# Kernel optimization log

Measured on AMD Instinct MI355X. Metric: run time of the kernel, lower is better.

## Reference

```python
import jax, jax.numpy as jnp
import numpy as np

N_NODES = 50000
N_EDGES = 400000
NODE_FEAT = 32
HIDDEN = 256
ACTION_DIM = 6
NUM_GRAPHS = 64


def setup_inputs() -> dict:
    key = jax.random.key(0)
    ks = jax.random.split(key, 9)
    x = jax.random.normal(ks[0], (N_NODES, NODE_FEAT), dtype=jnp.float32)
    edge_index = jax.random.randint(ks[1], (2, N_EDGES), 0, N_NODES, dtype=jnp.int32)
    batch = jnp.sort(jax.random.randint(ks[2], (N_NODES,), 0, NUM_GRAPHS, dtype=jnp.int32))
    # GCNConv weights (PyG stores Linear without bias + separate bias term;
    # here W is [in, out] so h = x @ W)
    s1 = 1.0 / np.sqrt(NODE_FEAT)
    s2 = 1.0 / np.sqrt(HIDDEN)
    W1 = jax.random.uniform(ks[3], (NODE_FEAT, HIDDEN), jnp.float32, -s1, s1)
    b1 = jnp.zeros((HIDDEN,), jnp.float32)
    W2 = jax.random.uniform(ks[4], (HIDDEN, HIDDEN), jnp.float32, -s2, s2)
    b2 = jnp.zeros((HIDDEN,), jnp.float32)
    Wf = jax.random.uniform(ks[5], (HIDDEN, 2 * ACTION_DIM), jnp.float32, -s2, s2)
    bf = jax.random.uniform(ks[6], (2 * ACTION_DIM,), jnp.float32, -s2, s2)
    return {"x": x, "edge_index": edge_index, "batch": batch,
            "W1": W1, "b1": b1, "W2": W2, "b2": b2, "Wf": Wf, "bf": bf}


def gcn_conv(x, src, dst, deg_inv_sqrt, W, b, num_nodes):
    # PyG GCNConv: h = x @ W, messages h[src] * norm scattered to dst, + bias.
    h = x @ W  # [N, out]
    norm = deg_inv_sqrt[src] * deg_inv_sqrt[dst]  # [E+N]
    msgs = h[src] * norm[:, None]  # [E+N, out]  (dominant memory traffic)
    out = jax.ops.segment_sum(msgs, dst, num_segments=num_nodes)
    return out + b


def reference(x, edge_index, batch, W1, b1, W2, b2, Wf, bf):
    num_nodes = x.shape[0]
    loop = jnp.arange(num_nodes, dtype=edge_index.dtype)
    src = jnp.concatenate([edge_index[0], loop])  # self-loops, PyG default
    dst = jnp.concatenate([edge_index[1], loop])
    deg = jax.ops.segment_sum(jnp.ones_like(dst, dtype=x.dtype), dst,
                              num_segments=num_nodes)  # >=1 due to self-loops
    deg_inv_sqrt = jax.lax.rsqrt(deg)

    h = jax.nn.relu(gcn_conv(x, src, dst, deg_inv_sqrt, W1, b1, num_nodes))
    h = jax.nn.relu(gcn_conv(h, src, dst, deg_inv_sqrt, W2, b2, num_nodes))

    # global_mean_pool over graph ids
    sums = jax.ops.segment_sum(h, batch, num_segments=NUM_GRAPHS)
    counts = jax.ops.segment_sum(jnp.ones((num_nodes,), x.dtype), batch,
                                 num_segments=NUM_GRAPHS)
    pooled = sums / jnp.maximum(counts, 1.0)[:, None]  # [G, HIDDEN]

    mls = pooled @ Wf + bf  # [G, 2*ACTION_DIM]
    mean, log_std = jnp.split(mls, 2, axis=-1)
    std = jnp.exp(jnp.clip(log_std, -20.0, 2.0))
    return mean, std
```

## Files before the change

kernel.cpp:

```cpp
#include <hip/hip_runtime.h>
#include <math.h>

#define NN 50000
#define FEAT 32
#define HID 256
#define NGRAPH 64
#define CAP 48

typedef __attribute__((ext_vector_type(8))) short bfrag;
typedef __attribute__((ext_vector_type(8))) unsigned short u16x8;
typedef __attribute__((ext_vector_type(4))) float f32x4;

__device__ __forceinline__ float bf2f(unsigned short u) {
    union { unsigned int i; float f; } v; v.i = ((unsigned int)u) << 16; return v.f;
}
__device__ __forceinline__ unsigned short f2bf(float f) {
    union { float f; unsigned int i; } v; v.f = f;
    unsigned int r = v.i + 0x7fffu + ((v.i >> 16) & 1u);
    return (unsigned short)(r >> 16);
}

__device__ __forceinline__ void pack_w(const float* __restrict__ W,
                                       unsigned short* __restrict__ Wp, int K, int o) {
    int j    = o & 7;
    int lane = (o >> 3) & 63;
    int rest = o >> 9;
    int nst  = K >> 5;
    int ks   = rest & (nst - 1);
    int nb   = rest / nst;
    int n = nb * 16 + (lane & 15);
    int k = ks * 32 + (lane >> 4) * 8 + j;
    Wp[o] = f2bf(W[(size_t)k * HID + n]);
}

__global__ void k_prep(float4* __restrict__ zp, int n16,
                       const float* __restrict__ W1, const float* __restrict__ W2,
                       unsigned short* __restrict__ W1p, unsigned short* __restrict__ W2p) {
    int i = blockIdx.x * blockDim.x + threadIdx.x;
    if (i < n16) zp[i] = make_float4(0.f, 0.f, 0.f, 0.f);
    if (i < FEAT * HID) pack_w(W1, W1p, FEAT, i);
    int o2 = i - FEAT * HID;
    if (o2 >= 0 && o2 < HID * HID) pack_w(W2, W2p, HID, o2);
}

__global__ void k_setup(const int* __restrict__ src, const int* __restrict__ dst,
                        const int* __restrict__ batch,
                        int* __restrict__ counter, unsigned short* __restrict__ csr,
                        int* __restrict__ starts, int E, int N) {
    int e = blockIdx.x * blockDim.x + threadIdx.x;
    if (e < E) {
        int d = dst[e];
        int p = atomicAdd(&counter[d], 1);
        if (p < CAP) csr[(size_t)d * CAP + p] = (unsigned short)src[e];
    }
    if (e < N) {
        int b = batch[e];
        int prev = (e == 0) ? -1 : batch[e - 1];
        if (b != prev) {
            for (int g = prev + 1; g <= b; ++g) starts[g] = e;
        }
        if (e == N - 1) {
            for (int g = b + 1; g <= NGRAPH; ++g) starts[g] = N;
        }
    }
}

__global__ void k_aggx(const float* __restrict__ x, const int* __restrict__ cnt,
                       const unsigned short* __restrict__ csr,
                       unsigned short* __restrict__ out, int N) {
    int node = blockIdx.x * 8 + (threadIdx.x >> 5);
    if (node >= N) return;
    int col = threadIdx.x & 31;
    int ecnt = cnt[node];
    float dn = rsqrtf((float)(ecnt + 1));
    int e = ecnt > CAP ? CAP : ecnt;
    const unsigned short* lst = &csr[(size_t)node * CAP];

    float acc = x[(size_t)node * FEAT + col] * dn;
    int i = 0;
    for (; i + 8 <= e; i += 8) {
        u16x8 s = *(const u16x8*)&lst[i];
        float vs[8];
#pragma unroll
        for (int j = 0; j < 8; ++j) {
            int sj = (int)s[j];
            vs[j] = x[(size_t)sj * FEAT + col] * rsqrtf((float)(cnt[sj] + 1));
        }
        acc += ((vs[0] + vs[1]) + (vs[2] + vs[3])) + ((vs[4] + vs[5]) + (vs[6] + vs[7]));
    }
    for (; i + 4 <= e; i += 4) {
        float vs[4];
#pragma unroll
        for (int j = 0; j < 4; ++j) {
            int sj = (int)lst[i + j];
            vs[j] = x[(size_t)sj * FEAT + col] * rsqrtf((float)(cnt[sj] + 1));
        }
        acc += (vs[0] + vs[1]) + (vs[2] + vs[3]);
    }
    for (; i < e; ++i) {
        int sj = (int)lst[i];
        acc += x[(size_t)sj * FEAT + col] * rsqrtf((float)(cnt[sj] + 1));
    }
    out[(size_t)node * FEAT + col] = f2bf(acc * dn);
}

__global__ void k_aggh(const unsigned short* __restrict__ hp, const int* __restrict__ cnt,
                       const unsigned short* __restrict__ csr,
                       unsigned short* __restrict__ outp, int N) {
    int panel = blockIdx.x & 7;
    int node = (blockIdx.x >> 3) * 64 + (threadIdx.x >> 2);
    if (node >= N) return;
    int c0 = (threadIdx.x & 3) * 8;
    const unsigned short* h = hp + (size_t)panel * N * 32;
    unsigned short* out = outp + (size_t)panel * N * 32;

    int ecnt = cnt[node];
    float dn = rsqrtf((float)(ecnt + 1));
    int e = ecnt > CAP ? CAP : ecnt;
    const unsigned short* lst = &csr[(size_t)node * CAP];

    bfrag sv = *(const bfrag*)&h[(size_t)node * 32 + c0];
    float a[8];
#pragma unroll
    for (int j = 0; j < 8; ++j) a[j] = bf2f((unsigned short)sv[j]);

    int i = 0;
    for (; i + 8 <= e; i += 8) {
        u16x8 s = *(const u16x8*)&lst[i];
        bfrag w0 = *(const bfrag*)&h[(size_t)s[0] * 32 + c0];
        bfrag w1 = *(const bfrag*)&h[(size_t)s[1] * 32 + c0];
        bfrag w2 = *(const bfrag*)&h[(size_t)s[2] * 32 + c0];
        bfrag w3 = *(const bfrag*)&h[(size_t)s[3] * 32 + c0];
        bfrag w4 = *(const bfrag*)&h[(size_t)s[4] * 32 + c0];
        bfrag w5 = *(const bfrag*)&h[(size_t)s[5] * 32 + c0];
        bfrag w6 = *(const bfrag*)&h[(size_t)s[6] * 32 + c0];
        bfrag w7 = *(const bfrag*)&h[(size_t)s[7] * 32 + c0];
#pragma unroll
        for (int j = 0; j < 8; ++j) {
            a[j] += ((bf2f((unsigned short)w0[j]) + bf2f((unsigned short)w1[j]))
                   + (bf2f((unsigned short)w2[j]) + bf2f((unsigned short)w3[j])))
                  + ((bf2f((unsigned short)w4[j]) + bf2f((unsigned short)w5[j]))
                   + (bf2f((unsigned short)w6[j]) + bf2f((unsigned short)w7[j])));
        }
    }
    for (; i + 4 <= e; i += 4) {
        bfrag w0 = *(const bfrag*)&h[(size_t)lst[i]     * 32 + c0];
        bfrag w1 = *(const bfrag*)&h[(size_t)lst[i + 1] * 32 + c0];
        bfrag w2 = *(const bfrag*)&h[(size_t)lst[i + 2] * 32 + c0];
        bfrag w3 = *(const bfrag*)&h[(size_t)lst[i + 3] * 32 + c0];
#pragma unroll
        for (int j = 0; j < 8; ++j)
            a[j] += (bf2f((unsigned short)w0[j]) + bf2f((unsigned short)w1[j]))
                  + (bf2f((unsigned short)w2[j]) + bf2f((unsigned short)w3[j]));
    }
    for (; i < e; ++i) {
        bfrag w = *(const bfrag*)&h[(size_t)lst[i] * 32 + c0];
#pragma unroll
        for (int j = 0; j < 8; ++j) a[j] += bf2f((unsigned short)w[j]);
    }
    bfrag o;
#pragma unroll
    for (int j = 0; j < 8; ++j) o[j] = (short)f2bf(a[j] * dn);
    *(bfrag*)&out[(size_t)node * 32 + c0] = o;
}

__global__ __launch_bounds__(256, 4)
void k_mmf(const unsigned short* __restrict__ A, const unsigned short* __restrict__ Wp,
           const float* __restrict__ bias, const int* __restrict__ cnt,
           unsigned short* __restrict__ C, int M) {
    __shared__ unsigned short lds[64 * 264];
    const int K = FEAT;
    int tid  = threadIdx.x;
    int lane = tid & 63;
    int wid  = tid >> 6;
    int l15  = lane & 15;
    int lq   = lane >> 4;
    int row0 = blockIdx.x * 64;

    const int P = K + 8;
    {
        int flat = tid * 8;
        int row = flat >> 5;
        int col = flat & 31;
        bfrag v = {0, 0, 0, 0, 0, 0, 0, 0};
        int gr = row0 + row;
        if (gr < M) v = *(const bfrag*)&A[(size_t)gr * K + col];
        *(bfrag*)&lds[row * P + col] = v;
    }
    __syncthreads();

    f32x4 acc[4][4];
#pragma unroll
    for (int mi = 0; mi < 4; ++mi)
#pragma unroll
        for (int ni = 0; ni < 4; ++ni) acc[mi][ni] = (f32x4){0.f, 0.f, 0.f, 0.f};

    bfrag fb[4];
#pragma unroll
    for (int ni = 0; ni < 4; ++ni) {
        size_t off = (((size_t)(wid * 4 + ni)) * 64 + lane) * 8;
        fb[ni] = *(const bfrag*)&Wp[off];
    }
    bfrag fa[4];
#pragma unroll
    for (int mi = 0; mi < 4; ++mi)
        fa[mi] = *(const bfrag*)&lds[(mi * 16 + l15) * P + lq * 8];
#pragma unroll
    for (int mi = 0; mi < 4; ++mi)
#pragma unroll
        for (int ni = 0; ni < 4; ++ni)
            acc[mi][ni] = __builtin_amdgcn_mfma_f32_16x16x32_bf16(fb[ni], fa[mi], acc[mi][ni], 0, 0, 0);

    float4 bv[4];
#pragma unroll
    for (int ni = 0; ni < 4; ++ni)
        bv[ni] = *(const float4*)&bias[(wid * 4 + ni) * 16 + lq * 4];
    float sv[4];
#pragma unroll
    for (int mi = 0; mi < 4; ++mi) {
        int gr = row0 + mi * 16 + l15;
        sv[mi] = (gr < M) ? rsqrtf((float)(cnt[gr] + 1)) : 0.f;
    }

    __syncthreads();
#pragma unroll
    for (int mi = 0; mi < 4; ++mi) {
#pragma unroll
        for (int ni = 0; ni < 4; ++ni) {
            const float* bp = (const float*)&bv[ni];
            ushort4 o;
            o.x = f2bf(fmaxf(acc[mi][ni][0] + bp[0], 0.f) * sv[mi]);
            o.y = f2bf(fmaxf(acc[mi][ni][1] + bp[1], 0.f) * sv[mi]);
            o.z = f2bf(fmaxf(acc[mi][ni][2] + bp[2], 0.f) * sv[mi]);
            o.w = f2bf(fmaxf(acc[mi][ni][3] + bp[3], 0.f) * sv[mi]);
            *(ushort4*)&lds[(mi * 16 + l15) * 264 + (wid * 4 + ni) * 16 + lq * 4] = o;
        }
    }
    __syncthreads();

#pragma unroll
    for (int i = 0; i < 8; ++i) {
        int F = (i * 256 + tid) * 8;
        int row = F >> 8;
        int col = F & 255;
        int gr = row0 + row;
        if (gr < M) {
            bfrag v = *(const bfrag*)&lds[row * 264 + col];
            *(bfrag*)&C[((size_t)(col >> 5) * M + gr) * 32 + (col & 31)] = v;
        }
    }
}

__global__ __launch_bounds__(256, 4)
void k_mmfp(const unsigned short* __restrict__ A, const unsigned short* __restrict__ Wp,
            const float* __restrict__ bias, const int* __restrict__ batch,
            float* __restrict__ pooled, int M) {
    __shared__ unsigned short lds[64 * 264];
    __shared__ int bshare[64];
    const int K = HID;
    int tid  = threadIdx.x;
    int lane = tid & 63;
    int wid  = tid >> 6;
    int l15  = lane & 15;
    int lq   = lane >> 4;
    int row0 = blockIdx.x * 64;

    if (tid < 64) {
        int gr = row0 + tid;
        bshare[tid] = (gr < M) ? batch[gr] : -1;
    }

    const int P = K + 8;
    for (int it = 0; it < 8; ++it) {
        int flat = (it * 256 + tid) * 8;
        int row = flat >> 8;
        int col = flat & 255;
        bfrag v = {0, 0, 0, 0, 0, 0, 0, 0};
        int gr = row0 + row;
        if (gr < M) v = *(const bfrag*)&A[((size_t)(col >> 5) * M + gr) * 32 + (col & 31)];
        *(bfrag*)&lds[row * P + col] = v;
    }
    __syncthreads();

    f32x4 acc[4][4];
#pragma unroll
    for (int mi = 0; mi < 4; ++mi)
#pragma unroll
        for (int ni = 0; ni < 4; ++ni) acc[mi][ni] = (f32x4){0.f, 0.f, 0.f, 0.f};

    for (int ks = 0; ks < 8; ++ks) {
        bfrag fb[4];
#pragma unroll
        for (int ni = 0; ni < 4; ++ni) {
            size_t off = (((size_t)(wid * 4 + ni) * 8 + ks) * 64 + lane) * 8;
            fb[ni] = *(const bfrag*)&Wp[off];
        }
        bfrag fa[4];
        int koff = ks * 32 + lq * 8;
#pragma unroll
        for (int mi = 0; mi < 4; ++mi)
            fa[mi] = *(const bfrag*)&lds[(mi * 16 + l15) * P + koff];
#pragma unroll
        for (int mi = 0; mi < 4; ++mi)
#pragma unroll
            for (int ni = 0; ni < 4; ++ni)
                acc[mi][ni] = __builtin_amdgcn_mfma_f32_16x16x32_bf16(fb[ni], fa[mi], acc[mi][ni], 0, 0, 0);
    }

    float4 bv[4];
#pragma unroll
    for (int ni = 0; ni < 4; ++ni)
        bv[ni] = *(const float4*)&bias[(wid * 4 + ni) * 16 + lq * 4];

    __syncthreads();
#pragma unroll
    for (int mi = 0; mi < 4; ++mi) {
#pragma unroll
        for (int ni = 0; ni < 4; ++ni) {
            const float* bp = (const float*)&bv[ni];
            ushort4 o;
            o.x = f2bf(fmaxf(acc[mi][ni][0] + bp[0], 0.f));
            o.y = f2bf(fmaxf(acc[mi][ni][1] + bp[1], 0.f));
            o.z = f2bf(fmaxf(acc[mi][ni][2] + bp[2], 0.f));
            o.w = f2bf(fmaxf(acc[mi][ni][3] + bp[3], 0.f));
            *(ushort4*)&lds[(mi * 16 + l15) * 264 + (wid * 4 + ni) * 16 + lq * 4] = o;
        }
    }
    __syncthreads();

    int c = tid;
    float pacc = 0.f;
    int cur = bshare[0];
    for (int r = 0; r < 64; ++r) {
        int g = bshare[r];
        if (g != cur) {
            if (cur >= 0) atomicAdd(&pooled[(size_t)cur * HID + c], pacc);
            pacc = 0.f; cur = g;
        }
        pacc += bf2f(lds[r * 264 + c]);
    }
    if (cur >= 0) atomicAdd(&pooled[(size_t)cur * HID + c], pacc);
}

__global__ void k_head(const float* __restrict__ pooled, const int* __restrict__ starts,
                       const float* __restrict__ Wf, const float* __restrict__ bf,
                       float* __restrict__ out) {
    int t = blockIdx.x * blockDim.x + threadIdx.x;
    if (t >= NGRAPH * 12) return;
    int g = t / 12, j = t % 12;
    float cntf = (float)(starts[g + 1] - starts[g]);
    float inv = 1.f / fmaxf(cntf, 1.f);
    float s = 0.f;
    for (int k = 0; k < HID; ++k) s += pooled[(size_t)g * HID + k] * Wf[k * 12 + j];
    s = s * inv + bf[j];
    if (j < 6) {
        out[g * 6 + j] = s;
    } else {
        float ls = fminf(fmaxf(s, -20.f), 2.f);
        out[NGRAPH * 6 + g * 6 + (j - 6)] = expf(ls);
    }
}

extern "C" void kernel_launch(void* const* d_in, const int* in_sizes, int n_in,
                              void* d_out, int out_size, void* d_ws, size_t ws_size,
                              hipStream_t stream) {
    const float* x     = (const float*)d_in[0];
    const int*   ei    = (const int*)d_in[1];
    const int*   batch = (const int*)d_in[2];
    const float* W1    = (const float*)d_in[3];
    const float* b1    = (const float*)d_in[4];
    const float* W2    = (const float*)d_in[5];
    const float* b2    = (const float*)d_in[6];
    const float* Wf    = (const float*)d_in[7];
    const float* bfv   = (const float*)d_in[8];
    float* out = (float*)d_out;

    const int E = in_sizes[1] / 2;
    const int N = in_sizes[2];
    const int* srcp = ei;
    const int* dstp = ei + E;

    char* ws = (char*)d_ws;
    const size_t OFF_CTR    = 0;
    const size_t OFF_POOLED = 200192;
    const size_t OFF_STARTS = 265728;
    const size_t OFF_W1P    = 266240;
    const size_t OFF_W2P    = 282624;
    const size_t OFF_CSR    = 413696;
    const size_t OFF_AGGX   = 5213696;
    const size_t OFF_H1     = 8413696;
    const size_t OFF_G      = 34013696;

    int*            ctr    = (int*)(ws + OFF_CTR);
    float*          pooled = (float*)(ws + OFF_POOLED);
    int*            starts = (int*)(ws + OFF_STARTS);
    unsigned short* W1p    = (unsigned short*)(ws + OFF_W1P);
    unsigned short* W2p    = (unsigned short*)(ws + OFF_W2P);
    unsigned short* csr    = (unsigned short*)(ws + OFF_CSR);
    unsigned short* aggX   = (unsigned short*)(ws + OFF_AGGX);
    unsigned short* h1     = (unsigned short*)(ws + OFF_H1);
    unsigned short* g      = (unsigned short*)(ws + OFF_G);

    const int T = 256;
    const int prep_n = (FEAT + HID) * HID;
    k_prep<<<(prep_n + T - 1) / T, T, 0, stream>>>((float4*)ws, 265728 / 16, W1, W2, W1p, W2p);
    k_setup<<<(E + T - 1) / T, T, 0, stream>>>(srcp, dstp, batch, ctr, csr, starts, E, N);

    k_aggx<<<(N + 7) / 8, T, 0, stream>>>(x, ctr, csr, aggX, N);
    k_mmf<<<(N + 63) / 64, T, 0, stream>>>(aggX, W1p, b1, ctr, h1, N);

    k_aggh<<<((N + 63) / 64) * 8, T, 0, stream>>>(h1, ctr, csr, g, N);
    k_mmfp<<<(N + 63) / 64, T, 0, stream>>>(g, W2p, b2, batch, pooled, N);

    k_head<<<3, T, 0, stream>>>(pooled, starts, Wf, bfv, out);
}
```

Baseline: 117.3 us.

## Reorder layer-2 to matmul-then-aggregate, fuse bias/relu/pool into aggregation, bf16 x

Layer 2 now runs the dense 256x256 matmul first and aggregates the transformed features afterward. The bias, ReLU and mean-pool atomics move into the aggregation kernel, so the aggregated hidden tensor is no longer written and re-read before pooling. The weight packing is moved from the zeroing kernel into the setup kernel, and x is converted once to bf16 there, halving gather traffic in the first aggregation. This adds an extra precision loss on x and another pass to convert it. The pool now issues atomics per 32-column panel, so there are more atomic launch points.

After: 131.7 us. 12.2% more time.

```diff
diff --git a/kernel.cpp b/kernel.cpp
--- a/kernel.cpp
+++ b/kernel.cpp
@@ -33,20 +33,18 @@
     Wp[o] = f2bf(W[(size_t)k * HID + n]);
 }
 
-__global__ void k_prep(float4* __restrict__ zp, int n16,
-                       const float* __restrict__ W1, const float* __restrict__ W2,
-                       unsigned short* __restrict__ W1p, unsigned short* __restrict__ W2p) {
+__global__ void k_prep(float4* __restrict__ zp, int n16) {
     int i = blockIdx.x * blockDim.x + threadIdx.x;
     if (i < n16) zp[i] = make_float4(0.f, 0.f, 0.f, 0.f);
-    if (i < FEAT * HID) pack_w(W1, W1p, FEAT, i);
-    int o2 = i - FEAT * HID;
-    if (o2 >= 0 && o2 < HID * HID) pack_w(W2, W2p, HID, o2);
 }
 
 __global__ void k_setup(const int* __restrict__ src, const int* __restrict__ dst,
-                        const int* __restrict__ batch,
+                        const int* __restrict__ batch, const float* __restrict__ x,
+                        const float* __restrict__ W1, const float* __restrict__ W2,
                         int* __restrict__ counter, unsigned short* __restrict__ csr,
-                        int* __restrict__ starts, int E, int N) {
+                        int* __restrict__ starts, unsigned short* __restrict__ xbf,
+                        unsigned short* __restrict__ W1p, unsigned short* __restrict__ W2p,
+                        int E, int N) {
     int e = blockIdx.x * blockDim.x + threadIdx.x;
     if (e < E) {
         int d = dst[e];
@@ -63,9 +61,15 @@
             for (int g = b + 1; g <= NGRAPH; ++g) starts[g] = N;
         }
     }
-}
-
-__global__ void k_aggx(const float* __restrict__ x, const int* __restrict__ cnt,
+    if (e < FEAT * HID) pack_w(W1, W1p, FEAT, e);
+    int o2 = e - FEAT * HID;
+    if (o2 >= 0 && o2 < HID * HID) pack_w(W2, W2p, HID, o2);
+    int total = N * FEAT;
+    int stride = gridDim.x * blockDim.x;
+    for (int i = e; i < total; i += stride) xbf[i] = f2bf(x[i]);
+}
+
+__global__ void k_aggx(const unsigned short* __restrict__ xbf, const int* __restrict__ cnt,
                        const unsigned short* __restrict__ csr,
                        unsigned short* __restrict__ out, int N) {
     int node = blockIdx.x * 8 + (threadIdx.x >> 5);
@@ -76,7 +80,7 @@
     int e = ecnt > CAP ? CAP : ecnt;
     const unsigned short* lst = &csr[(size_t)node * CAP];
 
-    float acc = x[(size_t)node * FEAT + col] * dn;
+    float acc = bf2f(xbf[(size_t)node * FEAT + col]) * dn;
     int i = 0;
     for (; i + 8 <= e; i += 8) {
         u16x8 s = *(const u16x8*)&lst[i];
@@ -84,7 +88,7 @@
 #pragma unroll
         for (int j = 0; j < 8; ++j) {
             int sj = (int)s[j];
-            vs[j] = x[(size_t)sj * FEAT + col] * rsqrtf((float)(cnt[sj] + 1));
+            vs[j] = bf2f(xbf[(size_t)sj * FEAT + col]) * rsqrtf((float)(cnt[sj] + 1));
         }
         acc += ((vs[0] + vs[1]) + (vs[2] + vs[3])) + ((vs[4] + vs[5]) + (vs[6] + vs[7]));
     }
@@ -93,75 +97,15 @@
 #pragma unroll
         for (int j = 0; j < 4; ++j) {
             int sj = (int)lst[i + j];
-            vs[j] = x[(size_t)sj * FEAT + col] * rsqrtf((float)(cnt[sj] + 1));
+            vs[j] = bf2f(xbf[(size_t)sj * FEAT + col]) * rsqrtf((float)(cnt[sj] + 1));
         }
         acc += (vs[0] + vs[1]) + (vs[2] + vs[3]);
     }
     for (; i < e; ++i) {
         int sj = (int)lst[i];
-        acc += x[(size_t)sj * FEAT + col] * rsqrtf((float)(cnt[sj] + 1));
+        acc += bf2f(xbf[(size_t)sj * FEAT + col]) * rsqrtf((float)(cnt[sj] + 1));
     }
     out[(size_t)node * FEAT + col] = f2bf(acc * dn);
-}
-
-__global__ void k_aggh(const unsigned short* __restrict__ hp, const int* __restrict__ cnt,
-                       const unsigned short* __restrict__ csr,
-                       unsigned short* __restrict__ outp, int N) {
-    int panel = blockIdx.x & 7;
-    int node = (blockIdx.x >> 3) * 64 + (threadIdx.x >> 2);
-    if (node >= N) return;
-    int c0 = (threadIdx.x & 3) * 8;
-    const unsigned short* h = hp + (size_t)panel * N * 32;
-    unsigned short* out = outp + (size_t)panel * N * 32;
-
-    int ecnt = cnt[node];
-    float dn = rsqrtf((float)(ecnt + 1));
-    int e = ecnt > CAP ? CAP : ecnt;
-    const unsigned short* lst = &csr[(size_t)node * CAP];
-
-    bfrag sv = *(const bfrag*)&h[(size_t)node * 32 + c0];
-    float a[8];
-#pragma unroll
-    for (int j = 0; j < 8; ++j) a[j] = bf2f((unsigned short)sv[j]);
-
-    int i = 0;
-    for (; i + 8 <= e; i += 8) {
-        u16x8 s = *(const u16x8*)&lst[i];
-        bfrag w0 = *(const bfrag*)&h[(size_t)s[0] * 32 + c0];
-        bfrag w1 = *(const bfrag*)&h[(size_t)s[1] * 32 + c0];
-        bfrag w2 = *(const bfrag*)&h[(size_t)s[2] * 32 + c0];
-        bfrag w3 = *(const bfrag*)&h[(size_t)s[3] * 32 + c0];
-        bfrag w4 = *(const bfrag*)&h[(size_t)s[4] * 32 + c0];
-        bfrag w5 = *(const bfrag*)&h[(size_t)s[5] * 32 + c0];
-        bfrag w6 = *(const bfrag*)&h[(size_t)s[6] * 32 + c0];
-        bfrag w7 = *(const bfrag*)&h[(size_t)s[7] * 32 + c0];
-#pragma unroll
-        for (int j = 0; j < 8; ++j) {
-            a[j] += ((bf2f((unsigned short)w0[j]) + bf2f((unsigned short)w1[j]))
-                   + (bf2f((unsigned short)w2[j]) + bf2f((unsigned short)w3[j])))
-                  + ((bf2f((unsigned short)w4[j]) + bf2f((unsigned short)w5[j]))
-                   + (bf2f((unsigned short)w6[j]) + bf2f((unsigned short)w7[j])));
-        }
-    }
-    for (; i + 4 <= e; i += 4) {
-        bfrag w0 = *(const bfrag*)&h[(size_t)lst[i]     * 32 + c0];
-        bfrag w1 = *(const bfrag*)&h[(size_t)lst[i + 1] * 32 + c0];
-        bfrag w2 = *(const bfrag*)&h[(size_t)lst[i + 2] * 32 + c0];
-        bfrag w3 = *(const bfrag*)&h[(size_t)lst[i + 3] * 32 + c0];
-#pragma unroll
-        for (int j = 0; j < 8; ++j)
-            a[j] += (bf2f((unsigned short)w0[j]) + bf2f((unsigned short)w1[j]))
-                  + (bf2f((unsigned short)w2[j]) + bf2f((unsigned short)w3[j]));
-    }
-    for (; i < e; ++i) {
-        bfrag w = *(const bfrag*)&h[(size_t)lst[i] * 32 + c0];
-#pragma unroll
-        for (int j = 0; j < 8; ++j) a[j] += bf2f((unsigned short)w[j]);
-    }
-    bfrag o;
-#pragma unroll
-    for (int j = 0; j < 8; ++j) o[j] = (short)f2bf(a[j] * dn);
-    *(bfrag*)&out[(size_t)node * 32 + c0] = o;
 }
 
 __global__ __launch_bounds__(256, 4)
@@ -252,11 +196,9 @@
 }
 
 __global__ __launch_bounds__(256, 4)
-void k_mmfp(const unsigned short* __restrict__ A, const unsigned short* __restrict__ Wp,
-            const float* __restrict__ bias, const int* __restrict__ batch,
-            float* __restrict__ pooled, int M) {
+void k_mm2(const unsigned short* __restrict__ A, const unsigned short* __restrict__ Wp,
+           unsigned short* __restrict__ T, int M) {
     __shared__ unsigned short lds[64 * 264];
-    __shared__ int bshare[64];
     const int K = HID;
     int tid  = threadIdx.x;
     int lane = tid & 63;
@@ -264,11 +206,6 @@
     int l15  = lane & 15;
     int lq   = lane >> 4;
     int row0 = blockIdx.x * 64;
-
-    if (tid < 64) {
-        int gr = row0 + tid;
-        bshare[tid] = (gr < M) ? batch[gr] : -1;
-    }
 
     const int P = K + 8;
     for (int it = 0; it < 8; ++it) {
@@ -307,39 +244,124 @@
                 acc[mi][ni] = __builtin_amdgcn_mfma_f32_16x16x32_bf16(fb[ni], fa[mi], acc[mi][ni], 0, 0, 0);
     }
 
-    float4 bv[4];
-#pragma unroll
-    for (int ni = 0; ni < 4; ++ni)
-        bv[ni] = *(const float4*)&bias[(wid * 4 + ni) * 16 + lq * 4];
-
     __syncthreads();
 #pragma unroll
     for (int mi = 0; mi < 4; ++mi) {
 #pragma unroll
         for (int ni = 0; ni < 4; ++ni) {
-            const float* bp = (const float*)&bv[ni];
             ushort4 o;
-            o.x = f2bf(fmaxf(acc[mi][ni][0] + bp[0], 0.f));
-            o.y = f2bf(fmaxf(acc[mi][ni][1] + bp[1], 0.f));
-            o.z = f2bf(fmaxf(acc[mi][ni][2] + bp[2], 0.f));
-            o.w = f2bf(fmaxf(acc[mi][ni][3] + bp[3], 0.f));
+            o.x = f2bf(acc[mi][ni][0]);
+            o.y = f2bf(acc[mi][ni][1]);
+            o.z = f2bf(acc[mi][ni][2]);
+            o.w = f2bf(acc[mi][ni][3]);
             *(ushort4*)&lds[(mi * 16 + l15) * 264 + (wid * 4 + ni) * 16 + lq * 4] = o;
         }
     }
     __syncthreads();
 
-    int c = tid;
-    float pacc = 0.f;
-    int cur = bshare[0];
-    for (int r = 0; r < 64; ++r) {
-        int g = bshare[r];
-        if (g != cur) {
-            if (cur >= 0) atomicAdd(&pooled[(size_t)cur * HID + c], pacc);
-            pacc = 0.f; cur = g;
-        }
-        pacc += bf2f(lds[r * 264 + c]);
-    }
-    if (cur >= 0) atomicAdd(&pooled[(size_t)cur * HID + c], pacc);
+#pragma unroll
+    for (int i = 0; i < 8; ++i) {
+        int F = (i * 256 + tid) * 8;
+        int row = F >> 8;
+        int col = F & 255;
+        int gr = row0 + row;
+        if (gr < M) {
+            bfrag v = *(const bfrag*)&lds[row * 264 + col];
+            *(bfrag*)&T[((size_t)(col >> 5) * M + gr) * 32 + (col & 31)] = v;
+        }
+    }
+}
+
+__global__ void k_aggpool(const unsigned short* __restrict__ tp, const int* __restrict__ cnt,
+                          const unsigned short* __restrict__ csr, const float* __restrict__ b2,
+                          const int* __restrict__ batch, float* __restrict__ pooled, int N) {
+    __shared__ unsigned short tile[64 * 32];
+    __shared__ int bshare[64];
+    int panel = blockIdx.x & 7;
+    int base = (blockIdx.x >> 3) * 64;
+    int g4 = threadIdx.x >> 2;
+    int cl = (threadIdx.x & 3) * 8;
+    int node = base + g4;
+
+    if (threadIdx.x < 64) {
+        int gr = base + threadIdx.x;
+        bshare[threadIdx.x] = (gr < N) ? batch[gr] : -1;
+    }
+
+    const unsigned short* t = tp + (size_t)panel * N * 32;
+    float a[8];
+#pragma unroll
+    for (int j = 0; j < 8; ++j) a[j] = 0.f;
+
+    if (node < N) {
+        int ecnt = cnt[node];
+        float dn = rsqrtf((float)(ecnt + 1));
+        int e = ecnt > CAP ? CAP : ecnt;
+        const unsigned short* lst = &csr[(size_t)node * CAP];
+
+        bfrag sv = *(const bfrag*)&t[(size_t)node * 32 + cl];
+#pragma unroll
+        for (int j = 0; j < 8; ++j) a[j] = bf2f((unsigned short)sv[j]);
+
+        int i = 0;
+        for (; i + 8 <= e; i += 8) {
+            u16x8 s = *(const u16x8*)&lst[i];
+            bfrag w0 = *(const bfrag*)&t[(size_t)s[0] * 32 + cl];
+            bfrag w1 = *(const bfrag*)&t[(size_t)s[1] * 32 + cl];
+            bfrag w2 = *(const bfrag*)&t[(size_t)s[2] * 32 + cl];
+            bfrag w3 = *(const bfrag*)&t[(size_t)s[3] * 32 + cl];
+            bfrag w4 = *(const bfrag*)&t[(size_t)s[4] * 32 + cl];
+            bfrag w5 = *(const bfrag*)&t[(size_t)s[5] * 32 + cl];
+            bfrag w6 = *(const bfrag*)&t[(size_t)s[6] * 32 + cl];
+            bfrag w7 = *(const bfrag*)&t[(size_t)s[7] * 32 + cl];
+#pragma unroll
+            for (int j = 0; j < 8; ++j) {
+                a[j] += ((bf2f((unsigned short)w0[j]) + bf2f((unsigned short)w1[j]))
+                       + (bf2f((unsigned short)w2[j]) + bf2f((unsigned short)w3[j])))
+                      + ((bf2f((unsigned short)w4[j]) + bf2f((unsigned short)w5[j]))
+                       + (bf2f((unsigned short)w6[j]) + bf2f((unsigned short)w7[j])));
+            }
+        }
+        for (; i + 4 <= e; i += 4) {
+            bfrag w0 = *(const bfrag*)&t[(size_t)lst[i]     * 32 + cl];
+            bfrag w1 = *(const bfrag*)&t[(size_t)lst[i + 1] * 32 + cl];
+            bfrag w2 = *(const bfrag*)&t[(size_t)lst[i + 2] * 32 + cl];
+            bfrag w3 = *(const bfrag*)&t[(size_t)lst[i + 3] * 32 + cl];
+#pragma unroll
+            for (int j = 0; j < 8; ++j)
+                a[j] += (bf2f((unsigned short)w0[j]) + bf2f((unsigned short)w1[j]))
+                      + (bf2f((unsigned short)w2[j]) + bf2f((unsigned short)w3[j]));
+        }
+        for (; i < e; ++i) {
+            bfrag w = *(const bfrag*)&t[(size_t)lst[i] * 32 + cl];
+#pragma unroll
+            for (int j = 0; j < 8; ++j) a[j] += bf2f((unsigned short)w[j]);
+        }
+#pragma unroll
+        for (int j = 0; j < 8; ++j)
+            a[j] = fmaxf(a[j] * dn + b2[panel * 32 + cl + j], 0.f);
+    }
+
+    bfrag o;
+#pragma unroll
+    for (int j = 0; j < 8; ++j) o[j] = (short)f2bf(a[j]);
+    *(bfrag*)&tile[g4 * 32 + cl] = o;
+    __syncthreads();
+
+    if (threadIdx.x < 32) {
+        int c = threadIdx.x;
+        float pacc = 0.f;
+        int cur = bshare[0];
+        for (int r = 0; r < 64; ++r) {
+            int gg = bshare[r];
+            if (gg != cur) {
+                if (cur >= 0) atomicAdd(&pooled[(size_t)cur * HID + panel * 32 + c], pacc);
+                pacc = 0.f; cur = gg;
+            }
+            pacc += bf2f(tile[r * 32 + c]);
+        }
+        if (cur >= 0) atomicAdd(&pooled[(size_t)cur * HID + panel * 32 + c], pacc);
+    }
 }
 
 __global__ void k_head(const float* __restrict__ pooled, const int* __restrict__ starts,
@@ -383,13 +405,15 @@
     char* ws = (char*)d_ws;
     const size_t OFF_CTR    = 0;
     const size_t OFF_POOLED = 200192;
+    const size_t ZERO_BYTES = 265728;
     const size_t OFF_STARTS = 265728;
     const size_t OFF_W1P    = 266240;
     const size_t OFF_W2P    = 282624;
     const size_t OFF_CSR    = 413696;
-    const size_t OFF_AGGX   = 5213696;
-    const size_t OFF_H1     = 8413696;
-    const size_t OFF_G      = 34013696;
+    const size_t OFF_XBF    = 5213696;
+    const size_t OFF_AGGX   = 8413696;
+    const size_t OFF_H1     = 11613696;
+    const size_t OFF_T      = 37213696;
 
     int*            ctr    = (int*)(ws + OFF_CTR);
     float*          pooled = (float*)(ws + OFF_POOLED);
@@ -397,20 +421,21 @@
     unsigned short* W1p    = (unsigned short*)(ws + OFF_W1P);
     unsigned short* W2p    = (unsigned short*)(ws + OFF_W2P);
     unsigned short* csr    = (unsigned short*)(ws + OFF_CSR);
+    unsigned short* xbf    = (unsigned short*)(ws + OFF_XBF);
     unsigned short* aggX   = (unsigned short*)(ws + OFF_AGGX);
     unsigned short* h1     = (unsigned short*)(ws + OFF_H1);
-    unsigned short* g      = (unsigned short*)(ws + OFF_G);
+    unsigned short* t      = (unsigned short*)(ws + OFF_T);
 
     const int T = 256;
-    const int prep_n = (FEAT + HID) * HID;
-    k_prep<<<(prep_n + T - 1) / T, T, 0, stream>>>((float4*)ws, 265728 / 16, W1, W2, W1p, W2p);
-    k_setup<<<(E + T - 1) / T, T, 0, stream>>>(srcp, dstp, batch, ctr, csr, starts, E, N);
-
-    k_aggx<<<(N + 7) / 8, T, 0, stream>>>(x, ctr, csr, aggX, N);
+    k_prep<<<(265728 / 16 + T - 1) / T, T, 0, stream>>>((float4*)ws, 265728 / 16);
+    k_setup<<<(E + T - 1) / T, T, 0, stream>>>(srcp, dstp, batch, x, W1, W2,
+                                               ctr, csr, starts, xbf, W1p, W2p, E, N);
+
+    k_aggx<<<(N + 7) / 8, T, 0, stream>>>(xbf, ctr, csr, aggX, N);
     k_mmf<<<(N + 63) / 64, T, 0, stream>>>(aggX, W1p, b1, ctr, h1, N);
 
-    k_aggh<<<((N + 63) / 64) * 8, T, 0, stream>>>(h1, ctr, csr, g, N);
-    k_mmfp<<<(N + 63) / 64, T, 0, stream>>>(g, W2p, b2, batch, pooled, N);
+    k_mm2<<<(N + 63) / 64, T, 0, stream>>>(h1, W2p, t, N);
+    k_aggpool<<<((N + 63) / 64) * 8, T, 0, stream>>>(t, ctr, csr, b2, batch, pooled, N);
 
     k_head<<<3, T, 0, stream>>>(pooled, starts, Wf, bfv, out);
 }
```
